# Kernel optimization log

Measured on AMD Instinct MI355X. Metric: run time of the kernel, lower is better.

## Reference

```python
import jax, jax.numpy as jnp
import numpy as np


def _log_g(x):
    # log of g(x) = where(x>=0, x+0.5, sigmoid(x)), computed stably in log space
    return jnp.where(x >= 0.0, jnp.log(jax.nn.relu(x) + 0.5), -jax.nn.softplus(-x))


def setup_inputs() -> dict:
    key = jax.random.key(0)
    k1, k2, k3, k4 = jax.random.split(key, 4)
    B, T, D, H = 4, 8192, 512, 512
    x = jax.random.normal(k1, (B, T, D), dtype=jnp.float32)
    h_prev = jax.random.uniform(k2, (B, 1, H), dtype=jnp.float32)  # positive: log(h0) taken
    W_h = jax.random.normal(k3, (H, D), dtype=jnp.float32) * (1.0 / np.sqrt(D))
    b_h = jnp.zeros((H,), dtype=jnp.float32)
    W_z = jax.random.normal(k4, (H, D), dtype=jnp.float32) * (1.0 / np.sqrt(D))
    b_z = jnp.zeros((H,), dtype=jnp.float32)
    return {"x": x, "h_prev": h_prev, "W_h": W_h, "b_h": b_h, "W_z": W_z, "b_z": b_z}


def reference(x, h_prev, W_h, b_h, W_z, b_z):
    # parallel (seq_len > 1) minGRU forward via Heinsen log-space scan
    k = jnp.einsum('btd,hd->bth', x, W_z) + b_z           # (B,T,H) gate pre-activation
    log_z = -jax.nn.softplus(-k)                          # log sigmoid(k)
    log_coeffs = -jax.nn.softplus(k)                      # log (1 - sigmoid(k))
    log_tilde_h = _log_g(jnp.einsum('btd,hd->bth', x, W_h) + b_h)
    log_h0 = jnp.log(h_prev)                              # (B,1,H)
    log_values = jnp.concatenate([log_h0, log_z + log_tilde_h], axis=1)  # (B,T+1,H)
    # a_star = [0, cumsum(log_coeffs)]
    a_star = jnp.pad(jnp.cumsum(log_coeffs, axis=1), ((0, 0), (1, 0), (0, 0)))
    log_h = a_star + jax.lax.cumlogsumexp(log_values - a_star, axis=1)
    h = jnp.exp(log_h)[:, 1:]                             # drop h0 -> (B,T,H)
    return h
```

## Files before the change

### kernel.cpp

```cpp
#include <hip/hip_runtime.h>
#include <hip/hip_bf16.h>
#include <stdint.h>

#define B_ 4
#define T_ 8192
#define D_ 512
#define H_ 512
#define M_ (B_ * T_)
#define CHUNK 64
#define NCHUNK (T_ / CHUNK)

typedef __attribute__((ext_vector_type(8))) short short8;
typedef __attribute__((ext_vector_type(4))) float floatx4;

__device__ __forceinline__ unsigned short f2bf(float f) {
    union { float f; unsigned int u; } v; v.f = f;
    unsigned int u = v.u;
    u += 0x7fffu + ((u >> 16) & 1u);
    return (unsigned short)(u >> 16);
}
__device__ __forceinline__ float bf_lo(unsigned int u) {
    union { unsigned int i; float f; } a; a.i = u << 16; return a.f;
}
__device__ __forceinline__ float bf_hi(unsigned int u) {
    union { unsigned int i; float f; } a; a.i = u & 0xffff0000u; return a.f;
}
__device__ __forceinline__ unsigned int pk_cd(float c, float d) {
    return (unsigned int)f2bf(c) | ((unsigned int)f2bf(d) << 16);
}

__global__ void conv_all(const float* __restrict__ x,
                         const float* __restrict__ Wz,
                         const float* __restrict__ Wh,
                         unsigned short* __restrict__ xbf,
                         unsigned short* __restrict__ Wf)
{
    const int X4 = M_ * D_ / 4;
    const int W4 = H_ * D_ / 4;
    int i = blockIdx.x * blockDim.x + threadIdx.x;
    const float* src; unsigned short* dst; int idx;
    if (i < X4)             { src = x;  dst = xbf;                  idx = i; }
    else if (i < X4 + W4)   { src = Wz; dst = Wf;                   idx = i - X4; }
    else if (i < X4 + 2*W4) { src = Wh; dst = Wf + (size_t)H_ * D_; idx = i - X4 - W4; }
    else return;
    float4 v = ((const float4*)src)[idx];
    ushort4 w; w.x = f2bf(v.x); w.y = f2bf(v.y); w.z = f2bf(v.z); w.w = f2bf(v.w);
    ((ushort4*)dst)[idx] = w;
}

__global__ __launch_bounds__(256, 2)
void gemm_cd(const unsigned short* __restrict__ xbf,
             const unsigned short* __restrict__ Wf,
             const float* __restrict__ bz, const float* __restrict__ bh,
             unsigned short* __restrict__ cd)
{
    __shared__ unsigned short lA[128 * 32];
    __shared__ unsigned short lZ[128 * 32];
    __shared__ unsigned short lH[128 * 32];

    const int tid  = threadIdx.x;
    const int lane = tid & 63;
    const int wave = tid >> 6;
    const int xcd  = blockIdx.x & 7;
    const int nblk = (blockIdx.x >> 3) & 3;
    const int mblk = xcd * 32 + (blockIdx.x >> 5);
    const int m0 = mblk * 128;
    const int n0 = nblk * 128;
    const int wm = (wave >> 1) * 64;
    const int wn = (wave & 1) * 64;
    const int l15  = lane & 15;
    const int quad = lane >> 4;

    const int srow = lane >> 2;
    const int sp   = lane & 3;

    floatx4 acc_z[4][4], acc_h[4][4];
    #pragma unroll
    for (int i = 0; i < 4; ++i)
        #pragma unroll
        for (int j = 0; j < 4; ++j) { acc_z[i][j] = (floatx4)0.0f; acc_h[i][j] = (floatx4)0.0f; }

    for (int kt = 0; kt < D_ / 32; ++kt) {
        const int kb = kt * 32;
        __syncthreads();
        #pragma unroll
        for (int r = 0; r < 2; ++r) {
            const int chunk = r * 4 + wave;
            const int row   = chunk * 16 + srow;
            const int kp    = sp ^ (row & 3);
            __builtin_amdgcn_global_load_lds(
                (const __attribute__((address_space(1))) unsigned int*)
                    (xbf + (size_t)(m0 + row) * D_ + kb + kp * 8),
                (__attribute__((address_space(3))) unsigned int*)(lA + chunk * 512),
                16, 0, 0);
            __builtin_amdgcn_global_load_lds(
                (const __attribute__((address_space(1))) unsigned int*)
                    (Wf + (size_t)(n0 + row) * D_ + kb + kp * 8),
                (__attribute__((address_space(3))) unsigned int*)(lZ + chunk * 512),
                16, 0, 0);
            __builtin_amdgcn_global_load_lds(
                (const __attribute__((address_space(1))) unsigned int*)
                    (Wf + (size_t)(512 + n0 + row) * D_ + kb + kp * 8),
                (__attribute__((address_space(3))) unsigned int*)(lH + chunk * 512),
                16, 0, 0);
        }
        __syncthreads();

        short8 af[4], zf[4], hf[4];
        #pragma unroll
        for (int i = 0; i < 4; ++i) {
            const int ra = wm + i * 16 + l15;
            af[i] = *(const short8*)&lA[ra * 32 + ((quad ^ (ra & 3)) * 8)];
            const int rb = wn + i * 16 + l15;
            zf[i] = *(const short8*)&lZ[rb * 32 + ((quad ^ (rb & 3)) * 8)];
            hf[i] = *(const short8*)&lH[rb * 32 + ((quad ^ (rb & 3)) * 8)];
        }
        #pragma unroll
        for (int i = 0; i < 4; ++i)
            #pragma unroll
            for (int j = 0; j < 4; ++j) {
                acc_z[i][j] = __builtin_amdgcn_mfma_f32_16x16x32_bf16(zf[j], af[i], acc_z[i][j], 0, 0, 0);
                acc_h[i][j] = __builtin_amdgcn_mfma_f32_16x16x32_bf16(hf[j], af[i], acc_h[i][j], 0, 0, 0);
            }
    }

    #pragma unroll
    for (int j = 0; j < 4; ++j) {
        const int hl = n0 + wn + j * 16 + quad * 4;
        const float4 bzv = *(const float4*)&bz[hl];
        const float4 bhv = *(const float4*)&bh[hl];
        #pragma unroll
        for (int i = 0; i < 4; ++i) {
            const int gm = m0 + wm + i * 16 + l15;
            uint4 w;
            #pragma unroll
            for (int r = 0; r < 4; ++r) {
                float kz = acc_z[i][j][r] + ((const float*)&bzv)[r];
                float hp = acc_h[i][j][r] + ((const float*)&bhv)[r];
                float c  = 1.0f / (1.0f + __expf(kz));
                float g  = (hp >= 0.0f) ? (hp + 0.5f) : (1.0f / (1.0f + __expf(-hp)));
                float d  = (1.0f - c) * g;
                ((unsigned int*)&w)[r] = pk_cd(c, d);
            }
            *(uint4*)&cd[((size_t)gm * H_ + hl) * 2] = w;
        }
    }
}

__global__ __launch_bounds__(256)
void chunk_scan(const unsigned short* __restrict__ cd,
                float* __restrict__ Cagg, float* __restrict__ Dagg)
{
    const int tid = threadIdx.x;
    const int j = blockIdx.x & (NCHUNK - 1);
    const int b = blockIdx.x >> 7;
    const unsigned short* base = cd + (size_t)(b * T_ + j * CHUNK) * (H_ * 2) + 4 * tid;
    float C0 = 1.f, C1 = 1.f, D0 = 0.f, D1 = 0.f;
    #pragma unroll 16
    for (int t = 0; t < CHUNK; ++t) {
        uint2 v = *(const uint2*)(base + (size_t)t * (H_ * 2));
        float c0 = bf_lo(v.x), d0 = bf_hi(v.x);
        float c1 = bf_lo(v.y), d1 = bf_hi(v.y);
        D0 = fmaf(c0, D0, d0);  C0 *= c0;
        D1 = fmaf(c1, D1, d1);  C1 *= c1;
    }
    size_t o = ((size_t)(b * NCHUNK + j)) * H_ + 2 * tid;
    *(float2*)&Cagg[o] = make_float2(C0, C1);
    *(float2*)&Dagg[o] = make_float2(D0, D1);
}

__global__ __launch_bounds__(64)
void interchunk(const float* __restrict__ h_prev,
                const float* __restrict__ Cagg,
                const float* __restrict__ Dagg,
                float* __restrict__ Hstart)
{
    const int flat = blockIdx.x * 64 + threadIdx.x;
    const int b = flat >> 9;
    const int h = flat & 511;
    float hs = h_prev[(size_t)b * H_ + h];
    #pragma unroll 16
    for (int j = 0; j < NCHUNK; ++j) {
        size_t o = ((size_t)(b * NCHUNK + j)) * H_ + h;
        Hstart[o] = hs;
        hs = fmaf(Cagg[o], hs, Dagg[o]);
    }
}

__global__ __launch_bounds__(256)
void apply_scan(const unsigned short* __restrict__ cd,
                const float* __restrict__ Hstart,
                float* __restrict__ out)
{
    const int tid = threadIdx.x;
    const int j = blockIdx.x & (NCHUNK - 1);
    const int b = blockIdx.x >> 7;
    float2 hs = *(const float2*)&Hstart[((size_t)(b * NCHUNK + j)) * H_ + 2 * tid];
    float h0 = hs.x, h1 = hs.y;
    const unsigned short* base = cd + (size_t)(b * T_ + j * CHUNK) * (H_ * 2) + 4 * tid;
    float* ob = out + (size_t)(b * T_ + j * CHUNK) * H_ + 2 * tid;
    #pragma unroll 8
    for (int t = 0; t < CHUNK; ++t) {
        uint2 v = *(const uint2*)(base + (size_t)t * (H_ * 2));
        h0 = fmaf(bf_lo(v.x), h0, bf_hi(v.x));
        h1 = fmaf(bf_lo(v.y), h1, bf_hi(v.y));
        *(float2*)(ob + (size_t)t * H_) = make_float2(h0, h1);
    }
}

extern "C" void kernel_launch(void* const* d_in, const int* in_sizes, int n_in,
                              void* d_out, int out_size, void* d_ws, size_t ws_size,
                              hipStream_t stream)
{
    const float* x      = (const float*)d_in[0];
    const float* h_prev = (const float*)d_in[1];
    const float* W_h    = (const float*)d_in[2];
    const float* b_h    = (const float*)d_in[3];
    const float* W_z    = (const float*)d_in[4];
    const float* b_z    = (const float*)d_in[5];
    float* out = (float*)d_out;

    unsigned short* xbf = (unsigned short*)d_out;

    char* ws = (char*)d_ws;
    unsigned short* cd = (unsigned short*)ws;
    size_t cd_bytes = (size_t)M_ * H_ * 2 * sizeof(unsigned short);
    unsigned short* Wf = (unsigned short*)(ws + cd_bytes);
    size_t wf_bytes = (size_t)2 * H_ * D_ * sizeof(unsigned short);
    float* Cagg   = (float*)(ws + cd_bytes + wf_bytes);
    float* Dagg   = Cagg + (size_t)B_ * NCHUNK * H_;
    float* Hstart = Dagg + (size_t)B_ * NCHUNK * H_;

    {
        int total = M_ * D_ / 4 + 2 * (H_ * D_ / 4);
        conv_all<<<dim3((total + 255) / 256), dim3(256), 0, stream>>>(x, W_z, W_h, xbf, Wf);
    }
    gemm_cd<<<dim3((M_ / 128) * (H_ / 128)), dim3(256), 0, stream>>>(
        xbf, Wf, b_z, b_h, cd);
    chunk_scan<<<dim3(B_ * NCHUNK), dim3(256), 0, stream>>>(cd, Cagg, Dagg);
    interchunk<<<dim3(32), dim3(64), 0, stream>>>(h_prev, Cagg, Dagg, Hstart);
    apply_scan<<<dim3(B_ * NCHUNK), dim3(256), 0, stream>>>(cd, Hstart, out);
}
```

Baseline: 210.2 us.

## Fuse per-segment scan reduction into GEMM epilogue with double-buffered LDS

The per-chunk scan reduction moves into the GEMM epilogue. Each block stages its c/d tile in LDS and every wave reduces a 32-step segment, which removes the separate chunk_scan kernel and its full re-read of cd. The GEMM output tile shrinks to 128x64 with a double-buffered LDS prefetch and occupancy 3, and segments become 32 long, so there are more inter-segment aggregates and a longer serial interseg loop. The change risks lower MFMA reuse per block and more serial work in interseg.

```diff
diff --git a/kernel.cpp b/kernel.cpp
--- a/kernel.cpp
+++ b/kernel.cpp
@@ -7,8 +7,8 @@
 #define D_ 512
 #define H_ 512
 #define M_ (B_ * T_)
-#define CHUNK 64
-#define NCHUNK (T_ / CHUNK)
+#define SEG 32
+#define NSEG (M_ / SEG)
 
 typedef __attribute__((ext_vector_type(8))) short short8;
 typedef __attribute__((ext_vector_type(4))) float floatx4;
@@ -48,90 +48,108 @@
     ((ushort4*)dst)[idx] = w;
 }
 
-__global__ __launch_bounds__(256, 2)
+#define LDSB 35840
+
+__global__ __launch_bounds__(256, 3)
 void gemm_cd(const unsigned short* __restrict__ xbf,
              const unsigned short* __restrict__ Wf,
              const float* __restrict__ bz, const float* __restrict__ bh,
-             unsigned short* __restrict__ cd)
-{
-    __shared__ unsigned short lA[128 * 32];
-    __shared__ unsigned short lZ[128 * 32];
-    __shared__ unsigned short lH[128 * 32];
+             unsigned int* __restrict__ cd,
+             float2* __restrict__ Sagg)
+{
+    __shared__ __align__(16) char smem[LDSB];
+    unsigned short* lds = (unsigned short*)smem;
+    unsigned int*   cdl = (unsigned int*)smem;
 
     const int tid  = threadIdx.x;
     const int lane = tid & 63;
     const int wave = tid >> 6;
     const int xcd  = blockIdx.x & 7;
-    const int nblk = (blockIdx.x >> 3) & 3;
-    const int mblk = xcd * 32 + (blockIdx.x >> 5);
+    const int nblk = (blockIdx.x >> 3) & 7;
+    const int mblk = xcd * 32 + (blockIdx.x >> 6);
     const int m0 = mblk * 128;
-    const int n0 = nblk * 128;
+    const int n0 = nblk * 64;
     const int wm = (wave >> 1) * 64;
-    const int wn = (wave & 1) * 64;
+    const int wn = (wave & 1) * 32;
     const int l15  = lane & 15;
     const int quad = lane >> 4;
-
     const int srow = lane >> 2;
     const int sp   = lane & 3;
 
-    floatx4 acc_z[4][4], acc_h[4][4];
+    #define STAGE(p, kt)                                                          \
+    {                                                                             \
+        const int kb = (kt) * 32;                                                 \
+        unsigned short* bb = lds + (p) * 8192;                                    \
+        _Pragma("unroll")                                                         \
+        for (int r = 0; r < 2; ++r) {                                             \
+            const int chunk = r * 4 + wave;                                       \
+            const int row   = chunk * 16 + srow;                                  \
+            const int kp    = sp ^ (row & 3);                                     \
+            __builtin_amdgcn_global_load_lds(                                     \
+                (const __attribute__((address_space(1))) unsigned int*)           \
+                    (xbf + (size_t)(m0 + row) * D_ + kb + kp * 8),                \
+                (__attribute__((address_space(3))) unsigned int*)(bb + chunk * 512),\
+                16, 0, 0);                                                        \
+        }                                                                         \
+        {                                                                         \
+            const int row = wave * 16 + srow;                                     \
+            const int kp  = sp ^ (row & 3);                                       \
+            __builtin_amdgcn_global_load_lds(                                     \
+                (const __attribute__((address_space(1))) unsigned int*)           \
+                    (Wf + (size_t)(n0 + row) * D_ + kb + kp * 8),                 \
+                (__attribute__((address_space(3))) unsigned int*)(bb + 4096 + wave * 512),\
+                16, 0, 0);                                                        \
+            __builtin_amdgcn_global_load_lds(                                     \
+                (const __attribute__((address_space(1))) unsigned int*)           \
+                    (Wf + (size_t)(512 + n0 + row) * D_ + kb + kp * 8),           \
+                (__attribute__((address_space(3))) unsigned int*)(bb + 6144 + wave * 512),\
+                16, 0, 0);                                                        \
+        }                                                                         \
+    }
+
+    floatx4 acc_z[4][2], acc_h[4][2];
     #pragma unroll
     for (int i = 0; i < 4; ++i)
         #pragma unroll
-        for (int j = 0; j < 4; ++j) { acc_z[i][j] = (floatx4)0.0f; acc_h[i][j] = (floatx4)0.0f; }
-
-    for (int kt = 0; kt < D_ / 32; ++kt) {
-        const int kb = kt * 32;
+        for (int j = 0; j < 2; ++j) { acc_z[i][j] = (floatx4)0.0f; acc_h[i][j] = (floatx4)0.0f; }
+
+    STAGE(0, 0);
+
+    for (int kt = 0; kt < 16; ++kt) {
         __syncthreads();
-        #pragma unroll
-        for (int r = 0; r < 2; ++r) {
-            const int chunk = r * 4 + wave;
-            const int row   = chunk * 16 + srow;
-            const int kp    = sp ^ (row & 3);
-            __builtin_amdgcn_global_load_lds(
-                (const __attribute__((address_space(1))) unsigned int*)
-                    (xbf + (size_t)(m0 + row) * D_ + kb + kp * 8),
-                (__attribute__((address_space(3))) unsigned int*)(lA + chunk * 512),
-                16, 0, 0);
-            __builtin_amdgcn_global_load_lds(
-                (const __attribute__((address_space(1))) unsigned int*)
-                    (Wf + (size_t)(n0 + row) * D_ + kb + kp * 8),
-                (__attribute__((address_space(3))) unsigned int*)(lZ + chunk * 512),
-                16, 0, 0);
-            __builtin_amdgcn_global_load_lds(
-                (const __attribute__((address_space(1))) unsigned int*)
-                    (Wf + (size_t)(512 + n0 + row) * D_ + kb + kp * 8),
-                (__attribute__((address_space(3))) unsigned int*)(lH + chunk * 512),
-                16, 0, 0);
-        }
-        __syncthreads();
-
-        short8 af[4], zf[4], hf[4];
+        const int base = (kt & 1) * 8192;
+        short8 af[4], zf[2], hf[2];
         #pragma unroll
         for (int i = 0; i < 4; ++i) {
             const int ra = wm + i * 16 + l15;
-            af[i] = *(const short8*)&lA[ra * 32 + ((quad ^ (ra & 3)) * 8)];
-            const int rb = wn + i * 16 + l15;
-            zf[i] = *(const short8*)&lZ[rb * 32 + ((quad ^ (rb & 3)) * 8)];
-            hf[i] = *(const short8*)&lH[rb * 32 + ((quad ^ (rb & 3)) * 8)];
-        }
+            af[i] = *(const short8*)&lds[base + ra * 32 + ((quad ^ (ra & 3)) * 8)];
+        }
+        #pragma unroll
+        for (int j = 0; j < 2; ++j) {
+            const int rb = wn + j * 16 + l15;
+            zf[j] = *(const short8*)&lds[base + 4096 + rb * 32 + ((quad ^ (rb & 3)) * 8)];
+            hf[j] = *(const short8*)&lds[base + 6144 + rb * 32 + ((quad ^ (rb & 3)) * 8)];
+        }
+        if (kt < 15) STAGE((kt + 1) & 1, kt + 1);
         #pragma unroll
         for (int i = 0; i < 4; ++i)
             #pragma unroll
-            for (int j = 0; j < 4; ++j) {
+            for (int j = 0; j < 2; ++j) {
                 acc_z[i][j] = __builtin_amdgcn_mfma_f32_16x16x32_bf16(zf[j], af[i], acc_z[i][j], 0, 0, 0);
                 acc_h[i][j] = __builtin_amdgcn_mfma_f32_16x16x32_bf16(hf[j], af[i], acc_h[i][j], 0, 0, 0);
             }
     }
 
+    __syncthreads();
+
     #pragma unroll
-    for (int j = 0; j < 4; ++j) {
-        const int hl = n0 + wn + j * 16 + quad * 4;
-        const float4 bzv = *(const float4*)&bz[hl];
-        const float4 bhv = *(const float4*)&bh[hl];
+    for (int j = 0; j < 2; ++j) {
+        const int hlb = wn + j * 16 + quad * 4;
+        const float4 bzv = *(const float4*)&bz[n0 + hlb];
+        const float4 bhv = *(const float4*)&bh[n0 + hlb];
         #pragma unroll
         for (int i = 0; i < 4; ++i) {
-            const int gm = m0 + wm + i * 16 + l15;
+            const int mloc = wm + i * 16 + l15;
             uint4 w;
             #pragma unroll
             for (int r = 0; r < 4; ++r) {
@@ -142,69 +160,62 @@
                 float d  = (1.0f - c) * g;
                 ((unsigned int*)&w)[r] = pk_cd(c, d);
             }
-            *(uint4*)&cd[((size_t)gm * H_ + hl) * 2] = w;
-        }
-    }
+            *(uint4*)&cd[(size_t)(m0 + mloc) * H_ + n0 + hlb] = w;
+            *(uint4*)&cdl[mloc * 68 + hlb] = w;
+        }
+    }
+
+    __syncthreads();
+
+    {
+        float C = 1.0f, Dv = 0.0f;
+        const int t0 = wave * 32;
+        #pragma unroll
+        for (int t = 0; t < 32; ++t) {
+            unsigned int u = cdl[(t0 + t) * 68 + lane];
+            float c = bf_lo(u), d = bf_hi(u);
+            Dv = fmaf(c, Dv, d);
+            C *= c;
+        }
+        Sagg[(size_t)((m0 >> 5) + wave) * H_ + n0 + lane] = make_float2(C, Dv);
+    }
+    #undef STAGE
 }
 
 __global__ __launch_bounds__(256)
-void chunk_scan(const unsigned short* __restrict__ cd,
-                float* __restrict__ Cagg, float* __restrict__ Dagg)
-{
-    const int tid = threadIdx.x;
-    const int j = blockIdx.x & (NCHUNK - 1);
-    const int b = blockIdx.x >> 7;
-    const unsigned short* base = cd + (size_t)(b * T_ + j * CHUNK) * (H_ * 2) + 4 * tid;
-    float C0 = 1.f, C1 = 1.f, D0 = 0.f, D1 = 0.f;
-    #pragma unroll 16
-    for (int t = 0; t < CHUNK; ++t) {
-        uint2 v = *(const uint2*)(base + (size_t)t * (H_ * 2));
-        float c0 = bf_lo(v.x), d0 = bf_hi(v.x);
-        float c1 = bf_lo(v.y), d1 = bf_hi(v.y);
-        D0 = fmaf(c0, D0, d0);  C0 *= c0;
-        D1 = fmaf(c1, D1, d1);  C1 *= c1;
-    }
-    size_t o = ((size_t)(b * NCHUNK + j)) * H_ + 2 * tid;
-    *(float2*)&Cagg[o] = make_float2(C0, C1);
-    *(float2*)&Dagg[o] = make_float2(D0, D1);
-}
-
-__global__ __launch_bounds__(64)
-void interchunk(const float* __restrict__ h_prev,
-                const float* __restrict__ Cagg,
-                const float* __restrict__ Dagg,
-                float* __restrict__ Hstart)
-{
-    const int flat = blockIdx.x * 64 + threadIdx.x;
+void interseg(const float* __restrict__ h_prev,
+              const float2* __restrict__ Sagg,
+              float* __restrict__ Hseg)
+{
+    const int flat = blockIdx.x * 256 + threadIdx.x;
     const int b = flat >> 9;
     const int h = flat & 511;
     float hs = h_prev[(size_t)b * H_ + h];
-    #pragma unroll 16
-    for (int j = 0; j < NCHUNK; ++j) {
-        size_t o = ((size_t)(b * NCHUNK + j)) * H_ + h;
-        Hstart[o] = hs;
-        hs = fmaf(Cagg[o], hs, Dagg[o]);
+    #pragma unroll 8
+    for (int s = 0; s < T_ / SEG; ++s) {
+        size_t o = (size_t)(b * (T_ / SEG) + s) * H_ + h;
+        Hseg[o] = hs;
+        float2 cdv = Sagg[o];
+        hs = fmaf(cdv.x, hs, cdv.y);
     }
 }
 
 __global__ __launch_bounds__(256)
-void apply_scan(const unsigned short* __restrict__ cd,
-                const float* __restrict__ Hstart,
+void apply_scan(const unsigned int* __restrict__ cd,
+                const float* __restrict__ Hseg,
                 float* __restrict__ out)
 {
-    const int tid = threadIdx.x;
-    const int j = blockIdx.x & (NCHUNK - 1);
-    const int b = blockIdx.x >> 7;
-    float2 hs = *(const float2*)&Hstart[((size_t)(b * NCHUNK + j)) * H_ + 2 * tid];
-    float h0 = hs.x, h1 = hs.y;
-    const unsigned short* base = cd + (size_t)(b * T_ + j * CHUNK) * (H_ * 2) + 4 * tid;
-    float* ob = out + (size_t)(b * T_ + j * CHUNK) * H_ + 2 * tid;
+    const int sg   = blockIdx.x >> 1;
+    const int half = blockIdx.x & 1;
+    const int h = half * 256 + threadIdx.x;
+    float hs = Hseg[(size_t)sg * H_ + h];
+    const unsigned int* base = cd + (size_t)sg * SEG * H_ + h;
+    float* ob = out + (size_t)sg * SEG * H_ + h;
     #pragma unroll 8
-    for (int t = 0; t < CHUNK; ++t) {
-        uint2 v = *(const uint2*)(base + (size_t)t * (H_ * 2));
-        h0 = fmaf(bf_lo(v.x), h0, bf_hi(v.x));
-        h1 = fmaf(bf_lo(v.y), h1, bf_hi(v.y));
-        *(float2*)(ob + (size_t)t * H_) = make_float2(h0, h1);
+    for (int t = 0; t < SEG; ++t) {
+        unsigned int u = base[(size_t)t * H_];
+        hs = fmaf(bf_lo(u), hs, bf_hi(u));
+        ob[(size_t)t * H_] = hs;
     }
 }
 
@@ -223,21 +234,19 @@
     unsigned short* xbf = (unsigned short*)d_out;
 
     char* ws = (char*)d_ws;
-    unsigned short* cd = (unsigned short*)ws;
-    size_t cd_bytes = (size_t)M_ * H_ * 2 * sizeof(unsigned short);
+    unsigned int* cd = (unsigned int*)ws;
+    size_t cd_bytes = (size_t)M_ * H_ * 4;
     unsigned short* Wf = (unsigned short*)(ws + cd_bytes);
     size_t wf_bytes = (size_t)2 * H_ * D_ * sizeof(unsigned short);
-    float* Cagg   = (float*)(ws + cd_bytes + wf_bytes);
-    float* Dagg   = Cagg + (size_t)B_ * NCHUNK * H_;
-    float* Hstart = Dagg + (size_t)B_ * NCHUNK * H_;
+    float2* Sagg = (float2*)(ws + cd_bytes + wf_bytes);
+    float*  Hseg = (float*)(ws + cd_bytes + wf_bytes + (size_t)NSEG * H_ * sizeof(float2));
 
     {
         int total = M_ * D_ / 4 + 2 * (H_ * D_ / 4);
         conv_all<<<dim3((total + 255) / 256), dim3(256), 0, stream>>>(x, W_z, W_h, xbf, Wf);
     }
-    gemm_cd<<<dim3((M_ / 128) * (H_ / 128)), dim3(256), 0, stream>>>(
-        xbf, Wf, b_z, b_h, cd);
-    chunk_scan<<<dim3(B_ * NCHUNK), dim3(256), 0, stream>>>(cd, Cagg, Dagg);
-    interchunk<<<dim3(32), dim3(64), 0, stream>>>(h_prev, Cagg, Dagg, Hstart);
-    apply_scan<<<dim3(B_ * NCHUNK), dim3(256), 0, stream>>>(cd, Hstart, out);
-}
+    gemm_cd<<<dim3((M_ / 128) * (H_ / 64)), dim3(256), 0, stream>>>(
+        xbf, Wf, b_z, b_h, cd, Sagg);
+    interseg<<<dim3(8), dim3(256), 0, stream>>>(h_prev, Sagg, Hseg);
+    apply_scan<<<dim3(NSEG * 2), dim3(256), 0, stream>>>(cd, Hseg, out);
+}
```

After: 213.8 us. About the same (+1.7%).
